# Kernel tuning notes

Hardware: AMD Instinct MI355X
Metric: run time of the kernel (lower is better)

The kernel has to match this reference:

```python
import jax, jax.numpy as jnp
import numpy as np

BN_EPS = 1e-5

def _bn(x, g, b):
    # BatchNorm1d, training-mode batch statistics
    mu = x.mean(axis=0)
    var = x.var(axis=0)
    return g * (x - mu) / jnp.sqrt(var + BN_EPS) + b

def setup_inputs() -> dict:
    key = jax.random.key(0)
    ks = jax.random.split(key, 10)
    B2, D_in, D1, DIMS, C = 16384, 1024, 512, 256, 40
    B = B2 // 2
    def w(k, shape, fan_in):
        return jax.random.normal(k, shape, jnp.float32) / np.float32(np.sqrt(fan_in))
    return {
        "lufeat": jax.random.normal(ks[0], (B2, D_in), jnp.float32),
        "llabel": jax.random.randint(ks[1], (B,), 0, C),
        "W1": w(ks[2], (D_in, D1), D_in), "b1": jnp.zeros(D1, jnp.float32),
        "W2": w(ks[3], (D1, DIMS), D1), "b2": jnp.zeros(DIMS, jnp.float32),
        "W3": w(ks[4], (DIMS + C, 256), DIMS + C), "b3": jnp.zeros(256, jnp.float32),
        "W4": w(ks[5], (256, 64), 256), "b4": jnp.zeros(64, jnp.float32),
        "W5": w(ks[6], (64, 1), 64), "b5": jnp.zeros(1, jnp.float32),
        "g1": jnp.ones(256, jnp.float32), "be1": jnp.zeros(256, jnp.float32),
        "g2": jnp.ones(64, jnp.float32), "be2": jnp.zeros(64, jnp.float32),
        "mbank0": jax.random.normal(ks[7], (C, DIMS), jnp.float32),
        "start0": jnp.zeros(C, jnp.float32),
    }

def reference(lufeat, llabel, W1, b1, W2, b2, W3, b3, W4, b4, W5, b5,
              g1, be1, g2, be2, mbank0, start0):
    B = lufeat.shape[0] // 2
    h = (lufeat @ W1 + b1) @ W2 + b2            # [2B, dims]
    h = h / jnp.linalg.norm(h, axis=1, keepdims=True)
    lfeat, ufeat = h[:B], h[B:]

    # Sequential per-sample memory-bank scatter/EMA update (detached feats)
    lf_sg = jax.lax.stop_gradient(lfeat)
    def step(carry, xs):
        start, mbank = carry
        lab, feat = xs
        row = jnp.where(start[lab] == 0, feat, 0.9 * mbank[lab] + 0.1 * feat)
        return (start.at[lab].set(1.0), mbank.at[lab].set(row)), None
    (_, mbank), _ = jax.lax.scan(step, (start0, mbank0), (llabel, lf_sg))
    mbank = jax.lax.stop_gradient(mbank)

    # cdist retrieval: [B, C] euclidean distances
    lm = jnp.linalg.norm(lfeat[:, None, :] - mbank[None, :, :], axis=-1)
    lscores = lm.min(axis=-1)
    um = jnp.linalg.norm(ufeat[:, None, :] - mbank[None, :, :], axis=-1)

    uf = jnp.concatenate([ufeat, um], axis=-1)   # [B, dims + C]
    u = jax.nn.relu(_bn(uf @ W3 + b3, g1, be1))
    u = jax.nn.relu(_bn(u @ W4 + b4, g2, be2))   # dropout = identity (eval)
    uscores = u @ W5 + b5                        # [B, 1]
    return lscores, uscores, mbank
```

## Files before the change

### kernel.cpp

```cpp
#include <hip/hip_runtime.h>
#include <hip/hip_bf16.h>
#include <stdint.h>

typedef __attribute__((ext_vector_type(4))) float f32x4;
typedef __attribute__((ext_vector_type(8))) short s16x8;
typedef __attribute__((ext_vector_type(4))) unsigned short u16x4;
typedef __attribute__((ext_vector_type(4))) int i32x4;

#define B2T 16384
#define BH 8192
#define DIN 1024
#define DD1 512
#define DIMS 256
#define NC 40
#define CAPS 2048

__device__ __forceinline__ unsigned short f2b(float f) {
  unsigned int u = __builtin_bit_cast(unsigned int, f);
  u += 0x7FFFu + ((u >> 16) & 1u);
  return (unsigned short)(u >> 16);
}

__device__ __forceinline__ float b2f(unsigned short u) {
  return __builtin_bit_cast(float, ((unsigned int)u) << 16);
}

__device__ __forceinline__ void gload16(const void* g, void* l) {
  __builtin_amdgcn_global_load_lds(
      (const __attribute__((address_space(1))) void*)g,
      (__attribute__((address_space(3))) void*)l, 16, 0, 0);
}

__global__ __launch_bounds__(256) void prep_all(const float* __restrict__ lufeat,
                                                unsigned short* __restrict__ lufeatH,
                                                const float* __restrict__ W1,
                                                const float* __restrict__ W2,
                                                const float* __restrict__ b1,
                                                const float* __restrict__ b2,
                                                const float* __restrict__ W3,
                                                const float* __restrict__ W4,
                                                unsigned short* __restrict__ WeffT,
                                                float* __restrict__ beff,
                                                unsigned short* __restrict__ W3T,
                                                unsigned short* __restrict__ W4T,
                                                float* __restrict__ statz) {
  __shared__ float W1s[32][36];
  __shared__ float W2sT[32][36];
  int b = blockIdx.x, t = threadIdx.x;
  if (b < 1024) {
#pragma unroll
    for (int i = 0; i < 8; ++i) {
      int idx = b * 16384 + i * 2048 + t * 8;
      f32x4 v0 = *(const f32x4*)(lufeat + idx);
      f32x4 v1 = *(const f32x4*)(lufeat + idx + 4);
      s16x8 p;
      p[0] = (short)f2b(v0[0]); p[1] = (short)f2b(v0[1]);
      p[2] = (short)f2b(v0[2]); p[3] = (short)f2b(v0[3]);
      p[4] = (short)f2b(v1[0]); p[5] = (short)f2b(v1[1]);
      p[6] = (short)f2b(v1[2]); p[7] = (short)f2b(v1[3]);
      *(s16x8*)(lufeatH + idx) = p;
    }
  } else if (b < 1280) {
    int bb = b - 1024;
    int k0 = (bb & 31) * 32, n0 = (bb >> 5) * 32;
    int nn = t & 31, kq = t >> 5;
    f32x4 acc = (f32x4){0.f, 0.f, 0.f, 0.f};
    for (int j0 = 0; j0 < DD1; j0 += 32) {
#pragma unroll
      for (int i = 0; i < 4; ++i) {
        int idx = t + 256 * i;
        int kk = idx >> 5, jj = idx & 31;
        W1s[kk][jj] = W1[(size_t)(k0 + kk) * DD1 + j0 + jj];
        W2sT[jj][kk] = W2[(size_t)(j0 + kk) * DIMS + n0 + jj];
      }
      __syncthreads();
#pragma unroll
      for (int jj4 = 0; jj4 < 8; ++jj4) {
        f32x4 w2 = *(const f32x4*)&W2sT[nn][jj4 * 4];
        f32x4 w1_0 = *(const f32x4*)&W1s[kq * 4 + 0][jj4 * 4];
        f32x4 w1_1 = *(const f32x4*)&W1s[kq * 4 + 1][jj4 * 4];
        f32x4 w1_2 = *(const f32x4*)&W1s[kq * 4 + 2][jj4 * 4];
        f32x4 w1_3 = *(const f32x4*)&W1s[kq * 4 + 3][jj4 * 4];
        acc[0] += w1_0[0] * w2[0] + w1_0[1] * w2[1] + w1_0[2] * w2[2] + w1_0[3] * w2[3];
        acc[1] += w1_1[0] * w2[0] + w1_1[1] * w2[1] + w1_1[2] * w2[2] + w1_1[3] * w2[3];
        acc[2] += w1_2[0] * w2[0] + w1_2[1] * w2[1] + w1_2[2] * w2[2] + w1_2[3] * w2[3];
        acc[3] += w1_3[0] * w2[0] + w1_3[1] * w2[1] + w1_3[2] * w2[2] + w1_3[3] * w2[3];
      }
      __syncthreads();
    }
    u16x4 pk = {f2b(acc[0]), f2b(acc[1]), f2b(acc[2]), f2b(acc[3])};
    *(u16x4*)(WeffT + (size_t)(n0 + nn) * DIN + k0 + kq * 4) = pk;
  } else if (b == 1280) {
    float a0 = 0.f, a1 = 0.f, a2 = 0.f, a3 = 0.f, a4 = 0.f, a5 = 0.f, a6 = 0.f, a7 = 0.f;
    for (int j = 0; j < DD1; j += 8) {
      a0 += b1[j + 0] * W2[(size_t)(j + 0) * DIMS + t];
      a1 += b1[j + 1] * W2[(size_t)(j + 1) * DIMS + t];
      a2 += b1[j + 2] * W2[(size_t)(j + 2) * DIMS + t];
      a3 += b1[j + 3] * W2[(size_t)(j + 3) * DIMS + t];
      a4 += b1[j + 4] * W2[(size_t)(j + 4) * DIMS + t];
      a5 += b1[j + 5] * W2[(size_t)(j + 5) * DIMS + t];
      a6 += b1[j + 6] * W2[(size_t)(j + 6) * DIMS + t];
      a7 += b1[j + 7] * W2[(size_t)(j + 7) * DIMS + t];
    }
    beff[t] = b2[t] + (((a0 + a1) + (a2 + a3)) + ((a4 + a5) + (a6 + a7)));
  } else if (b < 1601) {
    int idx = (b - 1281) * 256 + t;
    int n = idx / 320, k = idx - n * 320;
    float v = (k < 296) ? W3[(size_t)k * 256 + n] : 0.0f;
    W3T[(size_t)n * 320 + k] = f2b(v);
  } else if (b < 1665) {
    int idx = (b - 1601) * 256 + t;
    int n = idx >> 8, k = idx & 255;
    W4T[(size_t)n * 256 + k] = f2b(W4[(size_t)k * 64 + n]);
  } else {
    for (int i = t; i < 680; i += 256) statz[i] = 0.0f;
  }
}

__global__ __launch_bounds__(256) void gemm1_dma(
    const unsigned short* __restrict__ AH, const unsigned short* __restrict__ BT,
    const float* __restrict__ bias, float* __restrict__ C,
    unsigned short* __restrict__ uf) {
  __shared__ __align__(16) char A_s[2][4096];
  __shared__ __align__(16) char B_s[2][32768];
  __shared__ float rs[4][32];
  int t = threadIdx.x, m0 = blockIdx.x * 32;
  int w = t >> 6, lane = t & 63, q = lane >> 4, ln = lane & 15;
  f32x4 acc[2][4];
#pragma unroll
  for (int mi = 0; mi < 2; ++mi)
// ... 84 lines not shown
      int ribf = mi * 16 + q * 4 + r;
      float inv = rs[0][ribf];
      int grow = m0 + ribf;
#pragma unroll
      for (int ni = 0; ni < 4; ++ni) {
        int col = w * 64 + ni * 16 + ln;
        float nv = v[mi][ni][r] * inv;
        if (grow < BH)
          C[(size_t)grow * DIMS + col] = nv;
        else
          uf[(size_t)(grow - BH) * 320 + col] = f2b(nv);
      }
    }
}

template <int AMODE, int NB, int MI, int CW, int EPI, int K, int TPB>
__global__ __launch_bounds__(TPB) void gemm_core(
    const void* __restrict__ Aptr, int lda, const unsigned short* __restrict__ BT,
    const float* __restrict__ bias, float* __restrict__ C, int ldc,
    float* __restrict__ sums, float* __restrict__ ssqs,
    const float* __restrict__ bnsum, const float* __restrict__ bnssq,
    const float* __restrict__ bng, const float* __restrict__ bnbe,
    unsigned short* __restrict__ uf) {
  constexpr int NW = TPB / 64;
  constexpr int RG = NW / CW;
  constexpr int AR = RG * MI * 16;
  constexpr int ACH = AR * 8;
  constexpr int ABN = (ACH + TPB - 1) / TPB;
  constexpr int BBN = NB * 8 / TPB;
  constexpr int BBUF = NB * 128;
  constexpr int ALOADS = (AMODE == 1) ? ABN : 2 * ABN;
  constexpr bool UNIF = (ACH >= TPB);
  __shared__ __align__(16) short A_s[2][AR][72];
  __shared__ __align__(16) char B_s[2 * BBUF];
  __shared__ float rs[CW][AR];
  __shared__ float bsc_s[(AMODE == 2) ? 256 : 1];
  __shared__ float bsh_s[(AMODE == 2) ? 256 : 1];
  int t = threadIdx.x;
  int m0 = blockIdx.x * AR;
  int w = t >> 6, lane = t & 63, q = lane >> 4, ln = lane & 15;
  f32x4 acc[MI][4];
#pragma unroll
  for (int mi = 0; mi < MI; ++mi)
#pragma unroll
    for (int ni = 0; ni < 4; ++ni) acc[mi][ni] = (f32x4){0.f, 0.f, 0.f, 0.f};

  f32x4 pa0[ABN][2], pa1[ABN][2];
  s16x8 pab0[ABN], pab1[ABN];

  auto issue = [&](int kbase, f32x4 (&paX)[ABN][2], s16x8 (&pabX)[ABN]) {
    if (ACH >= TPB || t < ACH) {
#pragma unroll
      for (int i = 0; i < ABN; ++i) {
        int ch = t + TPB * i, row = ch >> 3, kp = (ch & 7) * 8;
        if constexpr (AMODE == 1) {
          const unsigned short* A = (const unsigned short*)Aptr;
          pabX[i] = *(const s16x8*)(A + (size_t)(m0 + row) * lda + kbase + kp);
        } else {
          const float* A = (const float*)Aptr;
          const f32x4* src = (const f32x4*)(A + (size_t)(m0 + row) * lda + kbase + kp);
          paX[i][0] = src[0];
          paX[i][1] = src[1];
        }
      }
    }
  };

  auto gloadB = [&](int kbase, int bufi) {
#pragma unroll
    for (int i = 0; i < BBN; ++i) {
      int ch = t + TPB * i;
      int n = ch >> 3, j = ch & 7;
      int ksw = (j ^ (n & 7)) * 8;
      gload16(BT + (size_t)n * K + kbase + ksw,
              B_s + bufi * BBUF + (w * 64 + TPB * i) * 16);
    }
  };

  auto stage = [&](int kk, int bufi, f32x4 (&paX)[ABN][2], s16x8 (&pabX)[ABN]) {
    if (ACH >= TPB || t < ACH) {
#pragma unroll
      for (int i = 0; i < ABN; ++i) {
        int ch = t + TPB * i, row = ch >> 3, kp = (ch & 7) * 8;
        if constexpr (AMODE == 1) {
          *(s16x8*)&A_s[bufi][row][kp] = pabX[i];
        } else {
          f32x4 v0 = paX[i][0], v1 = paX[i][1];
          if constexpr (AMODE == 2) {
            float vv[8] = {v0[0], v0[1], v0[2], v0[3], v1[0], v1[1], v1[2], v1[3]};
#pragma unroll
            for (int j = 0; j < 8; ++j) {
              int f = kk + kp + j;
              vv[j] = fmaxf(vv[j] * bsc_s[f] + bsh_s[f], 0.0f);
            }
            v0 = (f32x4){vv[0], vv[1], vv[2], vv[3]};
            v1 = (f32x4){vv[4], vv[5], vv[6], vv[7]};
          }
          s16x8 p;
          p[0] = (short)f2b(v0[0]); p[1] = (short)f2b(v0[1]);
          p[2] = (short)f2b(v0[2]); p[3] = (short)f2b(v0[3]);
          p[4] = (short)f2b(v1[0]); p[5] = (short)f2b(v1[1]);
          p[6] = (short)f2b(v1[2]); p[7] = (short)f2b(v1[3]);
          *(s16x8*)&A_s[bufi][row][kp] = p;
        }
      }
    }
  };

  auto compute = [&](int cur) {
#pragma unroll
    for (int k32 = 0; k32 < 64; k32 += 32) {
      s16x8 af[MI];
      int ab = (w / CW) * MI * 16;
#pragma unroll
      for (int mi = 0; mi < MI; ++mi)
        af[mi] = *(const s16x8*)&A_s[cur][ab + mi * 16 + ln][k32 + q * 8];
      int nb0 = (w % CW) * 64;
#pragma unroll
      for (int ni = 0; ni < 4; ++ni) {
        int brow = nb0 + ni * 16 + ln;
        int bb = (brow * 128 + (k32 + q * 8) * 2) ^ ((brow & 7) << 4);
        s16x8 bfr = *(const s16x8*)(B_s + cur * BBUF + bb);
#pragma unroll
        for (int mi = 0; mi < MI; ++mi)
          acc[mi][ni] = __builtin_amdgcn_mfma_f32_16x16x32_bf16(af[mi], bfr, acc[mi][ni], 0, 0, 0);
      }
    }
  };

  auto kbar = [&](bool keepA) {
    if constexpr (UNIF) {
      if (keepA)
        asm volatile("s_waitcnt vmcnt(%0) lgkmcnt(0)" ::"n"(ALOADS) : "memory");
      else
        asm volatile("s_waitcnt vmcnt(0) lgkmcnt(0)" ::: "memory");
      __builtin_amdgcn_s_barrier();
      __builtin_amdgcn_sched_barrier(0);
    } else {
      __syncthreads();
    }
  };

  if constexpr (AMODE == 2) {
    if (t < 256) {
      float mu = bnsum[t] * (1.0f / 8192.0f);
      float var = bnssq[t] * (1.0f / 8192.0f) - mu * mu;
      float sc = bng[t] * rsqrtf(var + 1e-5f);
      bsc_s[t] = sc;
      bsh_s[t] = bnbe[t] - mu * sc;
    }
    __syncthreads();
  }

  const int nst = K >> 6;
  issue(0, pa0, pab0);
  gloadB(0, 0);
  __builtin_amdgcn_sched_barrier(0);
  if (nst > 1) issue(64, pa1, pab1);
  stage(0, 0, pa0, pab0);
  kbar(nst > 1);

  for (int s = 0; s < nst; s += 2) {
    if (s + 1 < nst) gloadB((s + 1) << 6, 1);
    __builtin_amdgcn_sched_barrier(0);
    if (s + 2 < nst) issue((s + 2) << 6, pa0, pab0);
    compute(0);
    if (s + 1 < nst) stage((s + 1) << 6, 1, pa1, pab1);
    kbar(s + 2 < nst);
    if (s + 1 < nst) {
      if (s + 2 < nst) gloadB((s + 2) << 6, 0);
      __builtin_amdgcn_sched_barrier(0);
      if (s + 3 < nst) issue((s + 3) << 6, pa1, pab1);
      compute(1);
      if (s + 2 < nst) stage((s + 2) << 6, 0, pa0, pab0);
      kbar(s + 3 < nst);
    }
  }

  float v[MI][4][4];
#pragma unroll
  for (int mi = 0; mi < MI; ++mi)
#pragma unroll
    for (int ni = 0; ni < 4; ++ni) {
      float bv = bias[(w % CW) * 64 + ni * 16 + ln];
#pragma unroll
      for (int r = 0; r < 4; ++r) v[mi][ni][r] = acc[mi][ni][r] + bv;
    }

#pragma unroll
  for (int mi = 0; mi < MI; ++mi)
#pragma unroll
    for (int ni = 0; ni < 4; ++ni)
#pragma unroll
      for (int r = 0; r < 4; ++r) {
        int grow = m0 + (w / CW) * MI * 16 + mi * 16 + q * 4 + r;
        int col = (w % CW) * 64 + ni * 16 + ln;
        C[(size_t)grow * ldc + col] = v[mi][ni][r];
      }
  if constexpr (EPI == 2 || EPI == 3) {
#pragma unroll
    for (int ni = 0; ni < 4; ++ni) {
      float s = 0.f, s2 = 0.f;
#pragma unroll
      for (int mi = 0; mi < MI; ++mi)
#pragma unroll
        for (int r = 0; r < 4; ++r) {
          float x = v[mi][ni][r];
          s += x; s2 += x * x;
        }
      s += __shfl_xor(s, 16); s += __shfl_xor(s, 32);
      s2 += __shfl_xor(s2, 16); s2 += __shfl_xor(s2, 32);
      if (q == 0) {
        int col = (w % CW) * 64 + ni * 16 + ln;
        atomicAdd(&sums[col], s);
        atomicAdd(&ssqs[col], s2);
      }
    }
  }
}

__global__ __launch_bounds__(256) void bank_kernel(const int* __restrict__ llabel,
                                                   const float* __restrict__ Hn,
                                                   const float* __restrict__ mbank0,
                                                   const float* __restrict__ start0,
                                                   float* __restrict__ mbank_out,
                                                   float* __restrict__ msq) {
  __shared__ i32x4 lab4[BH / 4];
  __shared__ int idx_s[CAPS];
  __shared__ float redp[256];
  __shared__ int wcnt[4];
  int t = threadIdx.x, c = blockIdx.x >> 2, dq = blockIdx.x & 3;
  int w = t >> 6, lane = t & 63;
  const float l09 = -0.15200309344504997f;

  for (int i = t; i < BH / 4; i += 256) lab4[i] = ((const i32x4*)llabel)[i];
  __syncthreads();
  const int* lab_s = (const int*)lab4;

  int base0 = w * (BH / 4);
  int cnt = 0;
  for (int b = 0; b < BH / 4; b += 64)
    cnt += (int)__popcll(__ballot(lab_s[base0 + b + lane] == c));
  if (lane == 0) wcnt[w] = cnt;
  __syncthreads();
  int off = 0;
#pragma unroll
  for (int i = 0; i < 4; ++i)
    if (i < w) off += wcnt[i];
  int Ktot = wcnt[0] + wcnt[1] + wcnt[2] + wcnt[3];
  int running = off;
  for (int b = 0; b < BH / 4; b += 64) {
    bool hit = lab_s[base0 + b + lane] == c;
    unsigned long long mk = __ballot(hit);
    if (hit) {
      int pos = running + (int)__popcll(mk & ((1ull << lane) - 1ull));
      if (pos < CAPS) idx_s[pos] = base0 + b + lane;
    }
    running += (int)__popcll(mk);
  }
  __syncthreads();
  int K = Ktot < CAPS ? Ktot : CAPS;
  bool fresh = (start0[c] == 0.0f);
  int dcol = t & 63, rr = t >> 6;
  int d = dq * 64 + dcol;
  float p0 = 0.f, p1 = 0.f, p2 = 0.f, p3 = 0.f;
  if (K > 0) {
    float w0fold = fresh ? exp2f((float)K * l09) : 0.f;
    int m = rr;
    for (; m + 12 < K; m += 16) {
      float e = (float)(K - 1 - m);
      float wa = 0.1f * exp2f(e * l09) + (m == 0 ? w0fold : 0.f);
      p0 += wa * Hn[(size_t)idx_s[m] * DIMS + d];
      p1 += 0.1f * exp2f((e - 4.f) * l09) * Hn[(size_t)idx_s[m + 4] * DIMS + d];
      p2 += 0.1f * exp2f((e - 8.f) * l09) * Hn[(size_t)idx_s[m + 8] * DIMS + d];
      p3 += 0.1f * exp2f((e - 12.f) * l09) * Hn[(size_t)idx_s[m + 12] * DIMS + d];
    }
    for (; m < K; m += 4) {
      float wa = 0.1f * exp2f((float)(K - 1 - m) * l09) + (m == 0 ? w0fold : 0.f);
      p0 += wa * Hn[(size_t)idx_s[m] * DIMS + d];
    }
  }
  redp[rr * 64 + dcol] = (p0 + p1) + (p2 + p3);
  __syncthreads();
  if (t < 64) {
    int dd = dq * 64 + t;
    float out;
    if (K == 0) {
      out = mbank0[(size_t)c * DIMS + dd];
    } else {
      float base_v = fresh ? 0.f : exp2f((float)K * l09) * mbank0[(size_t)c * DIMS + dd];
      out = ((redp[t] + redp[64 + t]) + (redp[128 + t] + redp[192 + t])) + base_v;
    }
    mbank_out[(size_t)c * DIMS + dd] = out;
    float vv = out * out;
#pragma unroll
    for (int o = 32; o; o >>= 1) vv += __shfl_xor(vv, o);
    if (t == 0) atomicAdd(&msq[c], vv);
  }
}

__global__ __launch_bounds__(256) void dist_kernel(const float* __restrict__ Hn,
                                                   const float* __restrict__ mbank,
                                                   const float* __restrict__ msq,
                                                   float* __restrict__ lscores,
                                                   unsigned short* __restrict__ uf) {
  __shared__ float Ms[NC][260];
  __shared__ float Hs[32][260];
  __shared__ float msq_s[NC];
  int t = threadIdx.x;
  int r0 = blockIdx.x * 32;
  for (int e = t; e < NC * 64; e += 256) {
    int i = e >> 6, d0 = (e & 63) * 4;
    *(f32x4*)&Ms[i][d0] = *(const f32x4*)(mbank + (size_t)i * DIMS + d0);
  }
  if (r0 < BH) {
    for (int e = t; e < 32 * 64; e += 256) {
      int i = e >> 6, d0 = (e & 63) * 4;
      *(f32x4*)&Hs[i][d0] = *(const f32x4*)(Hn + (size_t)(r0 + i) * DIMS + d0);
    }
  } else {
    for (int e = t; e < 32 * 32; e += 256) {
      int i = e >> 5, d0 = (e & 31) * 8;
      s16x8 vb = *(const s16x8*)(uf + (size_t)(r0 - BH + i) * 320 + d0);
#pragma unroll
      for (int j = 0; j < 8; ++j) Hs[i][d0 + j] = b2f((unsigned short)vb[j]);
    }
  }
  if (t < NC) msq_s[t] = msq[t];
  __syncthreads();
  int r = t >> 3, c0 = (t & 7) * 5;
  float g0 = 0, g1 = 0, g2 = 0, g3 = 0, g4 = 0;
  for (int d = 0; d < DIMS; d += 4) {
    f32x4 f = *(const f32x4*)&Hs[r][d];
    f32x4 m0v = *(const f32x4*)&Ms[c0 + 0][d];
    f32x4 m1v = *(const f32x4*)&Ms[c0 + 1][d];
    f32x4 m2v = *(const f32x4*)&Ms[c0 + 2][d];
    f32x4 m3v = *(const f32x4*)&Ms[c0 + 3][d];
    f32x4 m4v = *(const f32x4*)&Ms[c0 + 4][d];
    g0 += f[0] * m0v[0] + f[1] * m0v[1] + f[2] * m0v[2] + f[3] * m0v[3];
    g1 += f[0] * m1v[0] + f[1] * m1v[1] + f[2] * m1v[2] + f[3] * m1v[3];
    g2 += f[0] * m2v[0] + f[1] * m2v[1] + f[2] * m2v[2] + f[3] * m2v[3];
    g3 += f[0] * m3v[0] + f[1] * m3v[1] + f[2] * m3v[2] + f[3] * m3v[3];
    g4 += f[0] * m4v[0] + f[1] * m4v[1] + f[2] * m4v[2] + f[3] * m4v[3];
  }
  int row = r0 + r;
  float d2[5];
  d2[0] = 1.0f + msq_s[c0 + 0] - 2.0f * g0;
  d2[1] = 1.0f + msq_s[c0 + 1] - 2.0f * g1;
  d2[2] = 1.0f + msq_s[c0 + 2] - 2.0f * g2;
  d2[3] = 1.0f + msq_s[c0 + 3] - 2.0f * g3;
  d2[4] = 1.0f + msq_s[c0 + 4] - 2.0f * g4;
  if (row < BH) {
    float mn = fminf(fminf(fminf(d2[0], d2[1]), fminf(d2[2], d2[3])), d2[4]);
    mn = fminf(mn, __shfl_xor(mn, 1, 8));
    mn = fminf(mn, __shfl_xor(mn, 2, 8));
    mn = fminf(mn, __shfl_xor(mn, 4, 8));
    if ((t & 7) == 0) lscores[row] = sqrtf(fmaxf(mn, 0.0f));
  } else {
    unsigned short* dst = uf + (size_t)(row - BH) * 320 + 256 + c0;
#pragma unroll
    for (int qq = 0; qq < 5; ++qq) dst[qq] = f2b(sqrtf(fmaxf(d2[qq], 0.0f)));
  }
}

__global__ __launch_bounds__(256) void uscore_bn(const float* __restrict__ y2,
                                                 const float* __restrict__ sums2,
                                                 const float* __restrict__ ssqs2,
                                                 const float* __restrict__ g2,
                                                 const float* __restrict__ be2,
                                                 const float* __restrict__ W5,
                                                 const float* __restrict__ b5,
                                                 float* __restrict__ out) {
  int t = threadIdx.x;
  int wv = t >> 6, lane = t & 63;
  int row = blockIdx.x * 4 + wv;
  float mu = sums2[lane] * (1.0f / 8192.0f);
  float var = ssqs2[lane] * (1.0f / 8192.0f) - mu * mu;
  float sc = g2[lane] * rsqrtf(var + 1e-5f);
  float sh = be2[lane] - mu * sc;
  float v = fmaxf(y2[(size_t)row * 64 + lane] * sc + sh, 0.0f) * W5[lane];
#pragma unroll
  for (int o = 32; o; o >>= 1) v += __shfl_xor(v, o);
  if (lane == 0) out[row] = v + b5[0];
}

extern "C" void kernel_launch(void* const* d_in, const int* in_sizes, int n_in,
                              void* d_out, int out_size, void* d_ws, size_t ws_size,
                              hipStream_t stream) {
  const float* lufeat = (const float*)d_in[0];
  const int* llabel = (const int*)d_in[1];
  const float* W1 = (const float*)d_in[2];
  const float* b1 = (const float*)d_in[3];
  const float* W2 = (const float*)d_in[4];
  const float* b2 = (const float*)d_in[5];
  const float* W3 = (const float*)d_in[6];
  const float* b3 = (const float*)d_in[7];
  const float* W4 = (const float*)d_in[8];
  const float* b4 = (const float*)d_in[9];
// ... 8 lines not shown

  char* ws = (char*)d_ws;
  unsigned short* WeffT = (unsigned short*)(ws + 0);
  float* Hraw = (float*)(ws + 524288);
  float* ybuf = (float*)(ws + 524288);
  float* y2 = (float*)(ws + 8912896);
  unsigned short* uf = (unsigned short*)(ws + 17301504);
  unsigned short* W3T = (unsigned short*)(ws + 22544384);
  unsigned short* W4T = (unsigned short*)(ws + 22708224);
  float* beff = (float*)(ws + 22740992);
  float* sums1 = (float*)(ws + 22742016);
  float* ssq1 = sums1 + 256;
  float* sums2 = ssq1 + 256;
  float* ssq2 = sums2 + 64;
  float* msq = (float*)(ws + 22744576);
  unsigned short* lufeatH = (unsigned short*)(ws + 25165824);

  float* lscores = (float*)d_out;
  float* uscores = lscores + 8192;
  float* mbank = uscores + 8192;

  prep_all<<<1666, 256, 0, stream>>>(lufeat, lufeatH, W1, W2, b1, b2, W3, W4,
                                     WeffT, beff, W3T, W4T, sums1);
  gemm1_dma<<<512, 256, 0, stream>>>(lufeatH, WeffT, beff, Hraw, uf);
  bank_kernel<<<160, 256, 0, stream>>>(llabel, Hraw, mbank0, start0, mbank, msq);
  dist_kernel<<<512, 256, 0, stream>>>(Hraw, mbank, msq, lscores, uf);
  gemm_core<1, 256, 1, 4, 2, 320, 512><<<256, 512, 0, stream>>>(
      uf, 320, W3T, b3, ybuf, 256,
      sums1, ssq1, nullptr, nullptr, nullptr, nullptr, nullptr);
  gemm_core<2, 64, 1, 1, 3, 256, 256><<<128, 256, 0, stream>>>(
      ybuf, 256, W4T, b4, y2, 64,
      sums2, ssq2, sums1, ssq1, g1, be1, nullptr);
  uscore_bn<<<2048, 256, 0, stream>>>(y2, sums2, ssq2, g2, be2, W5, b5, uscores);
}
```

Before: 238.2 us.

## Fuse post-GEMM stages into one persistent kernel with atomic flag barriers

Replaces the bank, distance, two GEMM and uscore launches with a single back_all kernel. Block ranges take on each stage and wait on global atomic counters that earlier-stage blocks increment after a release fence. The flags live in workspace and are zeroed by the enlarged statz clear in prep_all. This removes several launch gaps and tail effects, but it relies on earlier-stage blocks being scheduled before the waiting ones (deadlock risk), and the GEMM tiles are retuned with smaller M per block. The prep kernel is also reordered so the small weight-prep blocks are dispatched before the large bf16 conversion.

```diff
diff --git a/kernel.cpp b/kernel.cpp
--- a/kernel.cpp
+++ b/kernel.cpp
@@ -29,6 +29,21 @@
   __builtin_amdgcn_global_load_lds(
       (const __attribute__((address_space(1))) void*)g,
       (__attribute__((address_space(3))) void*)l, 16, 0, 0);
+}
+
+__device__ __forceinline__ void sig(unsigned* f) {
+  __builtin_amdgcn_fence(__ATOMIC_RELEASE, "agent");
+  __syncthreads();
+  if (threadIdx.x == 0)
+    __hip_atomic_fetch_add(f, 1u, __ATOMIC_RELAXED, __HIP_MEMORY_SCOPE_AGENT);
+}
+__device__ __forceinline__ void waitf(unsigned* f, unsigned n) {
+  if (threadIdx.x == 0) {
+    while (__hip_atomic_load(f, __ATOMIC_RELAXED, __HIP_MEMORY_SCOPE_AGENT) < n)
+      __builtin_amdgcn_s_sleep(32);
+  }
+  __syncthreads();
+  __builtin_amdgcn_fence(__ATOMIC_ACQUIRE, "agent");
 }
 
 __global__ __launch_bounds__(256) void prep_all(const float* __restrict__ lufeat,
@@ -47,22 +62,8 @@
   __shared__ float W1s[32][36];
   __shared__ float W2sT[32][36];
   int b = blockIdx.x, t = threadIdx.x;
-  if (b < 1024) {
-#pragma unroll
-    for (int i = 0; i < 8; ++i) {
-      int idx = b * 16384 + i * 2048 + t * 8;
-      f32x4 v0 = *(const f32x4*)(lufeat + idx);
-      f32x4 v1 = *(const f32x4*)(lufeat + idx + 4);
-      s16x8 p;
-      p[0] = (short)f2b(v0[0]); p[1] = (short)f2b(v0[1]);
-      p[2] = (short)f2b(v0[2]); p[3] = (short)f2b(v0[3]);
-      p[4] = (short)f2b(v1[0]); p[5] = (short)f2b(v1[1]);
-      p[6] = (short)f2b(v1[2]); p[7] = (short)f2b(v1[3]);
-      *(s16x8*)(lufeatH + idx) = p;
-    }
-  } else if (b < 1280) {
-    int bb = b - 1024;
-    int k0 = (bb & 31) * 32, n0 = (bb >> 5) * 32;
+  if (b < 256) {
+    int k0 = (b & 31) * 32, n0 = (b >> 5) * 32;
     int nn = t & 31, kq = t >> 5;
     f32x4 acc = (f32x4){0.f, 0.f, 0.f, 0.f};
     for (int j0 = 0; j0 < DD1; j0 += 32) {
@@ -90,7 +91,7 @@
     }
     u16x4 pk = {f2b(acc[0]), f2b(acc[1]), f2b(acc[2]), f2b(acc[3])};
     *(u16x4*)(WeffT + (size_t)(n0 + nn) * DIN + k0 + kq * 4) = pk;
-  } else if (b == 1280) {
+  } else if (b == 256) {
     float a0 = 0.f, a1 = 0.f, a2 = 0.f, a3 = 0.f, a4 = 0.f, a5 = 0.f, a6 = 0.f, a7 = 0.f;
     for (int j = 0; j < DD1; j += 8) {
       a0 += b1[j + 0] * W2[(size_t)(j + 0) * DIMS + t];
@@ -103,17 +104,31 @@
       a7 += b1[j + 7] * W2[(size_t)(j + 7) * DIMS + t];
     }
     beff[t] = b2[t] + (((a0 + a1) + (a2 + a3)) + ((a4 + a5) + (a6 + a7)));
-  } else if (b < 1601) {
-    int idx = (b - 1281) * 256 + t;
+  } else if (b < 577) {
+    int idx = (b - 257) * 256 + t;
     int n = idx / 320, k = idx - n * 320;
     float v = (k < 296) ? W3[(size_t)k * 256 + n] : 0.0f;
     W3T[(size_t)n * 320 + k] = f2b(v);
-  } else if (b < 1665) {
-    int idx = (b - 1601) * 256 + t;
+  } else if (b < 641) {
+    int idx = (b - 577) * 256 + t;
     int n = idx >> 8, k = idx & 255;
     W4T[(size_t)n * 256 + k] = f2b(W4[(size_t)k * 64 + n]);
+  } else if (b == 641) {
+    for (int i = t; i < 684; i += 256) statz[i] = 0.0f;
   } else {
-    for (int i = t; i < 680; i += 256) statz[i] = 0.0f;
+    size_t base = (size_t)(b - 642) * 16384 + (size_t)t * 8;
+#pragma unroll
+    for (int i = 0; i < 8; ++i) {
+      size_t idx = base + (size_t)i * 2048;
+      f32x4 v0 = *(const f32x4*)(lufeat + idx);
+      f32x4 v1 = *(const f32x4*)(lufeat + idx + 4);
+      s16x8 p;
+      p[0] = (short)f2b(v0[0]); p[1] = (short)f2b(v0[1]);
+      p[2] = (short)f2b(v0[2]); p[3] = (short)f2b(v0[3]);
+      p[4] = (short)f2b(v1[0]); p[5] = (short)f2b(v1[1]);
+      p[6] = (short)f2b(v1[2]); p[7] = (short)f2b(v1[3]);
+      *(s16x8*)(lufeatH + idx) = p;
+    }
   }
 }
 
@@ -228,374 +243,332 @@
     }
 }
 
-template <int AMODE, int NB, int MI, int CW, int EPI, int K, int TPB>
-__global__ __launch_bounds__(TPB) void gemm_core(
-    const void* __restrict__ Aptr, int lda, const unsigned short* __restrict__ BT,
-    const float* __restrict__ bias, float* __restrict__ C, int ldc,
-    float* __restrict__ sums, float* __restrict__ ssqs,
-    const float* __restrict__ bnsum, const float* __restrict__ bnssq,
-    const float* __restrict__ bng, const float* __restrict__ bnbe,
-    unsigned short* __restrict__ uf) {
-  constexpr int NW = TPB / 64;
-  constexpr int RG = NW / CW;
-  constexpr int AR = RG * MI * 16;
-  constexpr int ACH = AR * 8;
-  constexpr int ABN = (ACH + TPB - 1) / TPB;
-  constexpr int BBN = NB * 8 / TPB;
-  constexpr int BBUF = NB * 128;
-  constexpr int ALOADS = (AMODE == 1) ? ABN : 2 * ABN;
-  constexpr bool UNIF = (ACH >= TPB);
-  __shared__ __align__(16) short A_s[2][AR][72];
-  __shared__ __align__(16) char B_s[2 * BBUF];
-  __shared__ float rs[CW][AR];
-  __shared__ float bsc_s[(AMODE == 2) ? 256 : 1];
-  __shared__ float bsh_s[(AMODE == 2) ? 256 : 1];
-  int t = threadIdx.x;
-  int m0 = blockIdx.x * AR;
-  int w = t >> 6, lane = t & 63, q = lane >> 4, ln = lane & 15;
-  f32x4 acc[MI][4];
-#pragma unroll
-  for (int mi = 0; mi < MI; ++mi)
-#pragma unroll
-    for (int ni = 0; ni < 4; ++ni) acc[mi][ni] = (f32x4){0.f, 0.f, 0.f, 0.f};
-
-  f32x4 pa0[ABN][2], pa1[ABN][2];
-  s16x8 pab0[ABN], pab1[ABN];
-
-  auto issue = [&](int kbase, f32x4 (&paX)[ABN][2], s16x8 (&pabX)[ABN]) {
-    if (ACH >= TPB || t < ACH) {
-#pragma unroll
-      for (int i = 0; i < ABN; ++i) {
-        int ch = t + TPB * i, row = ch >> 3, kp = (ch & 7) * 8;
-        if constexpr (AMODE == 1) {
-          const unsigned short* A = (const unsigned short*)Aptr;
-          pabX[i] = *(const s16x8*)(A + (size_t)(m0 + row) * lda + kbase + kp);
-        } else {
-          const float* A = (const float*)Aptr;
-          const f32x4* src = (const f32x4*)(A + (size_t)(m0 + row) * lda + kbase + kp);
-          paX[i][0] = src[0];
-          paX[i][1] = src[1];
+__global__ __launch_bounds__(256) void back_all(
+    const int* llabel, const float* Hn, const float* mbank0, const float* start0,
+    float* mbank, float* msq, float* lscores, unsigned short* uf,
+    const unsigned short* W3T, const float* b3, float* ybuf,
+    float* sums1, float* ssq1, const float* g1, const float* be1,
+    const unsigned short* W4T, const float* b4, float* y2,
+    float* sums2, float* ssq2, const float* g2, const float* be2,
+    const float* W5, const float* b5, float* uscores, unsigned* flags) {
+  __shared__ __align__(16) char smem[75264];
+  const int bx = blockIdx.x, t = threadIdx.x;
+  const int w = t >> 6, lane = t & 63, q = lane >> 4, ln = lane & 15;
+  const float l09 = -0.15200309344504997f;
+
+  if (bx < 160) {
+    int c = bx >> 2, dq = bx & 3;
+    int* lab_s = (int*)smem;
+    int* idx_s = (int*)(smem + 32768);
+    float* redp = (float*)(smem + 40960);
+    int* wcnt = (int*)(smem + 41984);
+    for (int i = t; i < BH / 4; i += 256) ((i32x4*)lab_s)[i] = ((const i32x4*)llabel)[i];
+    __syncthreads();
+    int base0 = w * (BH / 4);
+    int cnt = 0;
+    for (int b = 0; b < BH / 4; b += 64)
+      cnt += (int)__popcll(__ballot(lab_s[base0 + b + lane] == c));
+    if (lane == 0) wcnt[w] = cnt;
+    __syncthreads();
+    int off = 0;
+#pragma unroll
+    for (int i = 0; i < 4; ++i)
+      if (i < w) off += wcnt[i];
+    int Ktot = wcnt[0] + wcnt[1] + wcnt[2] + wcnt[3];
+    int running = off;
+    for (int b = 0; b < BH / 4; b += 64) {
+      bool hit = lab_s[base0 + b + lane] == c;
+      unsigned long long mk = __ballot(hit);
+      if (hit) {
+        int pos = running + (int)__popcll(mk & ((1ull << lane) - 1ull));
+        if (pos < CAPS) idx_s[pos] = base0 + b + lane;
+      }
+      running += (int)__popcll(mk);
+    }
+    __syncthreads();
+    int K = Ktot < CAPS ? Ktot : CAPS;
+    bool fresh = (start0[c] == 0.0f);
+    int dcol = t & 63, rr = t >> 6;
+    int d = dq * 64 + dcol;
+    float p0 = 0.f, p1 = 0.f, p2 = 0.f, p3 = 0.f;
+    if (K > 0) {
+      float w0fold = fresh ? exp2f((float)K * l09) : 0.f;
+      int m = rr;
+      for (; m + 12 < K; m += 16) {
+        float e = (float)(K - 1 - m);
+        float wa = 0.1f * exp2f(e * l09) + (m == 0 ? w0fold : 0.f);
+        p0 += wa * Hn[(size_t)idx_s[m] * DIMS + d];
+        p1 += 0.1f * exp2f((e - 4.f) * l09) * Hn[(size_t)idx_s[m + 4] * DIMS + d];
+        p2 += 0.1f * exp2f((e - 8.f) * l09) * Hn[(size_t)idx_s[m + 8] * DIMS + d];
+        p3 += 0.1f * exp2f((e - 12.f) * l09) * Hn[(size_t)idx_s[m + 12] * DIMS + d];
+      }
+      for (; m < K; m += 4) {
+        float wa = 0.1f * exp2f((float)(K - 1 - m) * l09) + (m == 0 ? w0fold : 0.f);
+        p0 += wa * Hn[(size_t)idx_s[m] * DIMS + d];
+      }
+    }
+    redp[rr * 64 + dcol] = (p0 + p1) + (p2 + p3);
+    __syncthreads();
+    if (t < 64) {
+      int dd = dq * 64 + t;
+      float out;
+      if (K == 0) {
+        out = mbank0[(size_t)c * DIMS + dd];
+      } else {
+        float base_v = fresh ? 0.f : exp2f((float)K * l09) * mbank0[(size_t)c * DIMS + dd];
+        out = ((redp[t] + redp[64 + t]) + (redp[128 + t] + redp[192 + t])) + base_v;
+      }
+      mbank[(size_t)c * DIMS + dd] = out;
+      float vv = out * out;
+#pragma unroll
+      for (int o = 32; o; o >>= 1) vv += __shfl_xor(vv, o);
+      if (t == 0) atomicAdd(&msq[c], vv);
+    }
+    sig(flags + 0);
+  } else if (bx < 672) {
+    waitf(flags + 0, 160u);
+    int db = bx - 160;
+    float* Ms = (float*)smem;
+    float* Hs = (float*)(smem + 41600);
+    float* msq_s = (float*)(smem + 74880);
+    int r0 = db * 32;
+    for (int e = t; e < NC * 64; e += 256) {
+      int i = e >> 6, d0 = (e & 63) * 4;
+      *(f32x4*)&Ms[i * 260 + d0] = *(const f32x4*)(mbank + (size_t)i * DIMS + d0);
+    }
+    if (r0 < BH) {
+      for (int e = t; e < 32 * 64; e += 256) {
+        int i = e >> 6, d0 = (e & 63) * 4;
+        *(f32x4*)&Hs[i * 260 + d0] = *(const f32x4*)(Hn + (size_t)(r0 + i) * DIMS + d0);
+      }
+    } else {
+      for (int e = t; e < 32 * 32; e += 256) {
+        int i = e >> 5, d0 = (e & 31) * 8;
+        s16x8 vb = *(const s16x8*)(uf + (size_t)(r0 - BH + i) * 320 + d0);
+#pragma unroll
+        for (int j = 0; j < 8; ++j) Hs[i * 260 + d0 + j] = b2f((unsigned short)vb[j]);
+      }
+    }
+    if (t < NC) msq_s[t] = msq[t];
+    __syncthreads();
+    int r = t >> 3, c0 = (t & 7) * 5;
+    float g0 = 0, g1v = 0, g2v = 0, g3 = 0, g4 = 0;
+    for (int d = 0; d < DIMS; d += 4) {
+      f32x4 f = *(const f32x4*)&Hs[r * 260 + d];
+      f32x4 m0v = *(const f32x4*)&Ms[(c0 + 0) * 260 + d];
+      f32x4 m1v = *(const f32x4*)&Ms[(c0 + 1) * 260 + d];
+      f32x4 m2v = *(const f32x4*)&Ms[(c0 + 2) * 260 + d];
+      f32x4 m3v = *(const f32x4*)&Ms[(c0 + 3) * 260 + d];
+      f32x4 m4v = *(const f32x4*)&Ms[(c0 + 4) * 260 + d];
+      g0 += f[0] * m0v[0] + f[1] * m0v[1] + f[2] * m0v[2] + f[3] * m0v[3];
+      g1v += f[0] * m1v[0] + f[1] * m1v[1] + f[2] * m1v[2] + f[3] * m1v[3];
+      g2v += f[0] * m2v[0] + f[1] * m2v[1] + f[2] * m2v[2] + f[3] * m2v[3];
+      g3 += f[0] * m3v[0] + f[1] * m3v[1] + f[2] * m3v[2] + f[3] * m3v[3];
+      g4 += f[0] * m4v[0] + f[1] * m4v[1] + f[2] * m4v[2] + f[3] * m4v[3];
+    }
+    int row = r0 + r;
+    float d2[5];
+    d2[0] = 1.0f + msq_s[c0 + 0] - 2.0f * g0;
+    d2[1] = 1.0f + msq_s[c0 + 1] - 2.0f * g1v;
+    d2[2] = 1.0f + msq_s[c0 + 2] - 2.0f * g2v;
+    d2[3] = 1.0f + msq_s[c0 + 3] - 2.0f * g3;
+    d2[4] = 1.0f + msq_s[c0 + 4] - 2.0f * g4;
+    if (row < BH) {
+      float mn = fminf(fminf(fminf(d2[0], d2[1]), fminf(d2[2], d2[3])), d2[4]);
+      mn = fminf(mn, __shfl_xor(mn, 1, 8));
+      mn = fminf(mn, __shfl_xor(mn, 2, 8));
+      mn = fminf(mn, __shfl_xor(mn, 4, 8));
+      if ((t & 7) == 0) lscores[row] = sqrtf(fmaxf(mn, 0.0f));
+    } else {
+      unsigned short* dst = uf + (size_t)(row - BH) * 320 + 256 + c0;
+#pragma unroll
+      for (int qq = 0; qq < 5; ++qq) dst[qq] = f2b(sqrtf(fmaxf(d2[qq], 0.0f)));
+    }
+    sig(flags + 1);
+  } else if (bx < 1184) {
+    waitf(flags + 1, 512u);
+    int gb = bx - 672;
+    char* A_s = smem;
+    char* B_s = smem + 4096;
+    int m0 = gb * 16;
+    f32x4 acc[4];
+#pragma unroll
+    for (int ni = 0; ni < 4; ++ni) acc[ni] = (f32x4){0.f, 0.f, 0.f, 0.f};
+
+    auto dma = [&](int s, int bufi) {
+      int kb = s * 64;
+      if (t < 128) {
+        int row = t >> 3, j = t & 7;
+        gload16(uf + (size_t)(m0 + row) * 320 + kb + ((j ^ (row & 7)) * 8),
+                A_s + bufi * 2048 + t * 16);
+      }
+#pragma unroll
+      for (int i = 0; i < 8; ++i) {
+        int ch = t + 256 * i, n = ch >> 3, j = ch & 7;
+        gload16(W3T + (size_t)n * 320 + kb + ((j ^ (n & 7)) * 8),
+                B_s + bufi * 32768 + (w * 64 + 256 * i) * 16);
+      }
+    };
+    auto compute = [&](int bufi) {
+#pragma unroll
+      for (int k32 = 0; k32 < 64; k32 += 32) {
+        int koff = (k32 + q * 8) * 2;
+        int arow = ln;
+        s16x8 af = *(const s16x8*)(A_s + bufi * 2048 + ((arow * 128 + koff) ^ ((arow & 7) << 4)));
+        int nb0 = w * 64;
+#pragma unroll
+        for (int ni = 0; ni < 4; ++ni) {
+          int brow = nb0 + ni * 16 + ln;
+          s16x8 bfr = *(const s16x8*)(B_s + bufi * 32768 + ((brow * 128 + koff) ^ ((brow & 7) << 4)));
+          acc[ni] = __builtin_amdgcn_mfma_f32_16x16x32_bf16(af, bfr, acc[ni], 0, 0, 0);
         }
       }
-    }
-  };
-
-  auto gloadB = [&](int kbase, int bufi) {
-#pragma unroll
-    for (int i = 0; i < BBN; ++i) {
-      int ch = t + TPB * i;
-      int n = ch >> 3, j = ch & 7;
-      int ksw = (j ^ (n & 7)) * 8;
-      gload16(BT + (size_t)n * K + kbase + ksw,
-              B_s + bufi * BBUF + (w * 64 + TPB * i) * 16);
-    }
-  };
-
-  auto stage = [&](int kk, int bufi, f32x4 (&paX)[ABN][2], s16x8 (&pabX)[ABN]) {
-    if (ACH >= TPB || t < ACH) {
-#pragma unroll
-      for (int i = 0; i < ABN; ++i) {
-        int ch = t + TPB * i, row = ch >> 3, kp = (ch & 7) * 8;
-        if constexpr (AMODE == 1) {
-          *(s16x8*)&A_s[bufi][row][kp] = pabX[i];
-        } else {
-          f32x4 v0 = paX[i][0], v1 = paX[i][1];
-          if constexpr (AMODE == 2) {
-            float vv[8] = {v0[0], v0[1], v0[2], v0[3], v1[0], v1[1], v1[2], v1[3]};
-#pragma unroll
-            for (int j = 0; j < 8; ++j) {
-              int f = kk + kp + j;
-              vv[j] = fmaxf(vv[j] * bsc_s[f] + bsh_s[f], 0.0f);
-            }
-            v0 = (f32x4){vv[0], vv[1], vv[2], vv[3]};
-            v1 = (f32x4){vv[4], vv[5], vv[6], vv[7]};
-          }
-          s16x8 p;
-          p[0] = (short)f2b(v0[0]); p[1] = (short)f2b(v0[1]);
-          p[2] = (short)f2b(v0[2]); p[3] = (short)f2b(v0[3]);
-          p[4] = (short)f2b(v1[0]); p[5] = (short)f2b(v1[1]);
-          p[6] = (short)f2b(v1[2]); p[7] = (short)f2b(v1[3]);
-          *(s16x8*)&A_s[bufi][row][kp] = p;
-        }
-      }
-    }
-  };
-
-  auto compute = [&](int cur) {
-#pragma unroll
-    for (int k32 = 0; k32 < 64; k32 += 32) {
-      s16x8 af[MI];
-      int ab = (w / CW) * MI * 16;
-#pragma unroll
-      for (int mi = 0; mi < MI; ++mi)
-        af[mi] = *(const s16x8*)&A_s[cur][ab + mi * 16 + ln][k32 + q * 8];
-      int nb0 = (w % CW) * 64;
-#pragma unroll
-      for (int ni = 0; ni < 4; ++ni) {
-        int brow = nb0 + ni * 16 + ln;
-        int bb = (brow * 128 + (k32 + q * 8) * 2) ^ ((brow & 7) << 4);
-        s16x8 bfr = *(const s16x8*)(B_s + cur * BBUF + bb);
-#pragma unroll
-        for (int mi = 0; mi < MI; ++mi)
-          acc[mi][ni] = __builtin_amdgcn_mfma_f32_16x16x32_bf16(af[mi], bfr, acc[mi][ni], 0, 0, 0);
-      }
-    }
-  };
-
-  auto kbar = [&](bool keepA) {
-    if constexpr (UNIF) {
-      if (keepA)
-        asm volatile("s_waitcnt vmcnt(%0) lgkmcnt(0)" ::"n"(ALOADS) : "memory");
-      else
-        asm volatile("s_waitcnt vmcnt(0) lgkmcnt(0)" ::: "memory");
-      __builtin_amdgcn_s_barrier();
-      __builtin_amdgcn_sched_barrier(0);
-    } else {
+    };
+    dma(0, 0);
+    __syncthreads();
+    for (int s = 0; s < 5; ++s) {
+      if (s + 1 < 5) dma(s + 1, (s + 1) & 1);
+      compute(s & 1);
       __syncthreads();
     }
-  };
-
-  if constexpr (AMODE == 2) {
-    if (t < 256) {
-      float mu = bnsum[t] * (1.0f / 8192.0f);
-      float var = bnssq[t] * (1.0f / 8192.0f) - mu * mu;
-      float sc = bng[t] * rsqrtf(var + 1e-5f);
-      bsc_s[t] = sc;
-      bsh_s[t] = bnbe[t] - mu * sc;
-    }
-    __syncthreads();
-  }
-
-  const int nst = K >> 6;
-  issue(0, pa0, pab0);
-  gloadB(0, 0);
-  __builtin_amdgcn_sched_barrier(0);
-  if (nst > 1) issue(64, pa1, pab1);
-  stage(0, 0, pa0, pab0);
-  kbar(nst > 1);
-
-  for (int s = 0; s < nst; s += 2) {
-    if (s + 1 < nst) gloadB((s + 1) << 6, 1);
-    __builtin_amdgcn_sched_barrier(0);
-    if (s + 2 < nst) issue((s + 2) << 6, pa0, pab0);
-    compute(0);
-    if (s + 1 < nst) stage((s + 1) << 6, 1, pa1, pab1);
-    kbar(s + 2 < nst);
-    if (s + 1 < nst) {
-      if (s + 2 < nst) gloadB((s + 2) << 6, 0);
-      __builtin_amdgcn_sched_barrier(0);
-      if (s + 3 < nst) issue((s + 3) << 6, pa1, pab1);
-      compute(1);
-      if (s + 2 < nst) stage((s + 2) << 6, 0, pa0, pab0);
-      kbar(s + 3 < nst);
-    }
-  }
-
-  float v[MI][4][4];
-#pragma unroll
-  for (int mi = 0; mi < MI; ++mi)
 #pragma unroll
     for (int ni = 0; ni < 4; ++ni) {
-      float bv = bias[(w % CW) * 64 + ni * 16 + ln];
-#pragma unroll
-      for (int r = 0; r < 4; ++r) v[mi][ni][r] = acc[mi][ni][r] + bv;
-    }
-
-#pragma unroll
-  for (int mi = 0; mi < MI; ++mi)
-#pragma unroll
-    for (int ni = 0; ni < 4; ++ni)
+      int col = w * 64 + ni * 16 + ln;
+      float bv = b3[col];
+      float s = 0.f, s2 = 0.f;
 #pragma unroll
       for (int r = 0; r < 4; ++r) {
-        int grow = m0 + (w / CW) * MI * 16 + mi * 16 + q * 4 + r;
-        int col = (w % CW) * 64 + ni * 16 + ln;
-        C[(size_t)grow * ldc + col] = v[mi][ni][r];
-      }
-  if constexpr (EPI == 2 || EPI == 3) {
-#pragma unroll
-    for (int ni = 0; ni < 4; ++ni) {
-      float s = 0.f, s2 = 0.f;
-#pragma unroll
-      for (int mi = 0; mi < MI; ++mi)
-#pragma unroll
-        for (int r = 0; r < 4; ++r) {
-          float x = v[mi][ni][r];
-          s += x; s2 += x * x;
-        }
+        float x = acc[ni][r] + bv;
+        ybuf[(size_t)(m0 + q * 4 + r) * 256 + col] = x;
+        s += x; s2 += x * x;
+      }
       s += __shfl_xor(s, 16); s += __shfl_xor(s, 32);
       s2 += __shfl_xor(s2, 16); s2 += __shfl_xor(s2, 32);
       if (q == 0) {
-        int col = (w % CW) * 64 + ni * 16 + ln;
-        atomicAdd(&sums[col], s);
-        atomicAdd(&ssqs[col], s2);
-      }
+        atomicAdd(&sums1[col], s);
+        atomicAdd(&ssq1[col], s2);
+      }
+    }
+    sig(flags + 2);
+  } else if (bx < 1312) {
+    waitf(flags + 2, 512u);
+    int hb = bx - 1184;
+    short* A3 = (short*)smem;
+    char* B3 = smem + 18432;
+    float* bsc = (float*)(smem + 34816);
+    float* bsh = (float*)(smem + 35840);
+    {
+      float mu = sums1[t] * (1.0f / 8192.0f);
+      float var = ssq1[t] * (1.0f / 8192.0f) - mu * mu;
+      float sc = g1[t] * rsqrtf(var + 1e-5f);
+      bsc[t] = sc;
+      bsh[t] = be1[t] - mu * sc;
+    }
+    __syncthreads();
+    int m0 = hb * 64;
+    f32x4 acc[4];
+#pragma unroll
+    for (int ni = 0; ni < 4; ++ni) acc[ni] = (f32x4){0.f, 0.f, 0.f, 0.f};
+    f32x4 pa0[2][2], pa1[2][2];
+    auto issueA3 = [&](int kbase, f32x4 (&pa)[2][2]) {
+#pragma unroll
+      for (int i = 0; i < 2; ++i) {
+        int ch = t + 256 * i, row = ch >> 3, kp = (ch & 7) * 8;
+        const f32x4* src = (const f32x4*)(ybuf + (size_t)(m0 + row) * 256 + kbase + kp);
+        pa[i][0] = src[0];
+        pa[i][1] = src[1];
+      }
+    };
+    auto stageA3 = [&](int kbase, int bufi, f32x4 (&pa)[2][2]) {
+#pragma unroll
+      for (int i = 0; i < 2; ++i) {
+        int ch = t + 256 * i, row = ch >> 3, kp = (ch & 7) * 8;
+        float vv[8] = {pa[i][0][0], pa[i][0][1], pa[i][0][2], pa[i][0][3],
+                       pa[i][1][0], pa[i][1][1], pa[i][1][2], pa[i][1][3]};
+#pragma unroll
+        for (int j = 0; j < 8; ++j) {
+          int f = kbase + kp + j;
+          vv[j] = fmaxf(vv[j] * bsc[f] + bsh[f], 0.0f);
+        }
+        s16x8 p;
+        p[0] = (short)f2b(vv[0]); p[1] = (short)f2b(vv[1]);
+        p[2] = (short)f2b(vv[2]); p[3] = (short)f2b(vv[3]);
+        p[4] = (short)f2b(vv[4]); p[5] = (short)f2b(vv[5]);
+        p[6] = (short)f2b(vv[6]); p[7] = (short)f2b(vv[7]);
+        *(s16x8*)&A3[(bufi * 64 + row) * 72 + kp] = p;
+      }
+    };
+    auto gloadB3 = [&](int kbase, int bufi) {
+#pragma unroll
+      for (int i = 0; i < 2; ++i) {
+        int ch = t + 256 * i, n = ch >> 3, j = ch & 7;
+        gload16(W4T + (size_t)n * 256 + kbase + ((j ^ (n & 7)) * 8),
+                B3 + bufi * 8192 + ch * 16);
+      }
+    };
+    auto compute3 = [&](int cur) {
+#pragma unroll
+      for (int k32 = 0; k32 < 64; k32 += 32) {
+        s16x8 af = *(const s16x8*)&A3[(cur * 64 + w * 16 + ln) * 72 + k32 + q * 8];
+#pragma unroll
+        for (int ni = 0; ni < 4; ++ni) {
+          int brow = ni * 16 + ln;
+          int bb = (brow * 128 + (k32 + q * 8) * 2) ^ ((brow & 7) << 4);
+          s16x8 bfr = *(const s16x8*)(B3 + cur * 8192 + bb);
+          acc[ni] = __builtin_amdgcn_mfma_f32_16x16x32_bf16(af, bfr, acc[ni], 0, 0, 0);
+        }
+      }
+    };
+    issueA3(0, pa0);
+    gloadB3(0, 0);
+    stageA3(0, 0, pa0);
+    issueA3(64, pa1);
+    __syncthreads();
+    for (int s = 0; s < 4; ++s) {
+      int cur = s & 1;
+      if (s + 1 < 4) gloadB3((s + 1) << 6, cur ^ 1);
+      if (s + 2 < 4) issueA3((s + 2) << 6, (s & 1) ? pa1 : pa0);
+      compute3(cur);
+      if (s + 1 < 4) stageA3((s + 1) << 6, cur ^ 1, (s & 1) ? pa0 : pa1);
+      __syncthreads();
+    }
+#pragma unroll
+    for (int ni = 0; ni < 4; ++ni) {
+      int col = ni * 16 + ln;
+      float bv = b4[col];
+      float s = 0.f, s2 = 0.f;
+#pragma unroll
+      for (int r = 0; r < 4; ++r) {
+        float x = acc[ni][r] + bv;
+        y2[(size_t)(m0 + w * 16 + q * 4 + r) * 64 + col] = x;
+        s += x; s2 += x * x;
+      }
+      s += __shfl_xor(s, 16); s += __shfl_xor(s, 32);
+      s2 += __shfl_xor(s2, 16); s2 += __shfl_xor(s2, 32);
+      if (q == 0) {
+        atomicAdd(&sums2[col], s);
+        atomicAdd(&ssq2[col], s2);
+      }
+    }
+    sig(flags + 3);
+  } else {
+    waitf(flags + 3, 128u);
+    int ub = bx - 1312;
+    float mu = sums2[lane] * (1.0f / 8192.0f);
+    float var = ssq2[lane] * (1.0f / 8192.0f) - mu * mu;
+    float sc = g2[lane] * rsqrtf(var + 1e-5f);
+    float sh = be2[lane] - mu * sc;
+    float w5 = W5[lane];
+    float bb5 = b5[0];
+#pragma unroll
+    for (int i = 0; i < 4; ++i) {
+      int row = ub * 16 + i * 4 + w;
+      float v = fmaxf(y2[(size_t)row * 64 + lane] * sc + sh, 0.0f) * w5;
+#pragma unroll
+      for (int o = 32; o; o >>= 1) v += __shfl_xor(v, o);
+      if (lane == 0) uscores[row] = v + bb5;
     }
   }
-}
-
-__global__ __launch_bounds__(256) void bank_kernel(const int* __restrict__ llabel,
-                                                   const float* __restrict__ Hn,
-                                                   const float* __restrict__ mbank0,
-                                                   const float* __restrict__ start0,
-                                                   float* __restrict__ mbank_out,
-                                                   float* __restrict__ msq) {
-  __shared__ i32x4 lab4[BH / 4];
-  __shared__ int idx_s[CAPS];
-  __shared__ float redp[256];
-  __shared__ int wcnt[4];
-  int t = threadIdx.x, c = blockIdx.x >> 2, dq = blockIdx.x & 3;
-  int w = t >> 6, lane = t & 63;
-  const float l09 = -0.15200309344504997f;
-
-  for (int i = t; i < BH / 4; i += 256) lab4[i] = ((const i32x4*)llabel)[i];
-  __syncthreads();
-  const int* lab_s = (const int*)lab4;
-
-  int base0 = w * (BH / 4);
-  int cnt = 0;
-  for (int b = 0; b < BH / 4; b += 64)
-    cnt += (int)__popcll(__ballot(lab_s[base0 + b + lane] == c));
-  if (lane == 0) wcnt[w] = cnt;
-  __syncthreads();
-  int off = 0;
-#pragma unroll
-  for (int i = 0; i < 4; ++i)
-    if (i < w) off += wcnt[i];
-  int Ktot = wcnt[0] + wcnt[1] + wcnt[2] + wcnt[3];
-  int running = off;
-  for (int b = 0; b < BH / 4; b += 64) {
-    bool hit = lab_s[base0 + b + lane] == c;
-    unsigned long long mk = __ballot(hit);
-    if (hit) {
-      int pos = running + (int)__popcll(mk & ((1ull << lane) - 1ull));
-      if (pos < CAPS) idx_s[pos] = base0 + b + lane;
-    }
-    running += (int)__popcll(mk);
-  }
-  __syncthreads();
-  int K = Ktot < CAPS ? Ktot : CAPS;
-  bool fresh = (start0[c] == 0.0f);
-  int dcol = t & 63, rr = t >> 6;
-  int d = dq * 64 + dcol;
-  float p0 = 0.f, p1 = 0.f, p2 = 0.f, p3 = 0.f;
-  if (K > 0) {
-    float w0fold = fresh ? exp2f((float)K * l09) : 0.f;
-    int m = rr;
-    for (; m + 12 < K; m += 16) {
-      float e = (float)(K - 1 - m);
-      float wa = 0.1f * exp2f(e * l09) + (m == 0 ? w0fold : 0.f);
-      p0 += wa * Hn[(size_t)idx_s[m] * DIMS + d];
-      p1 += 0.1f * exp2f((e - 4.f) * l09) * Hn[(size_t)idx_s[m + 4] * DIMS + d];
-      p2 += 0.1f * exp2f((e - 8.f) * l09) * Hn[(size_t)idx_s[m + 8] * DIMS + d];
-      p3 += 0.1f * exp2f((e - 12.f) * l09) * Hn[(size_t)idx_s[m + 12] * DIMS + d];
-    }
-    for (; m < K; m += 4) {
-      float wa = 0.1f * exp2f((float)(K - 1 - m) * l09) + (m == 0 ? w0fold : 0.f);
-      p0 += wa * Hn[(size_t)idx_s[m] * DIMS + d];
-    }
-  }
-  redp[rr * 64 + dcol] = (p0 + p1) + (p2 + p3);
-  __syncthreads();
-  if (t < 64) {
-    int dd = dq * 64 + t;
-    float out;
-    if (K == 0) {
-      out = mbank0[(size_t)c * DIMS + dd];
-    } else {
-      float base_v = fresh ? 0.f : exp2f((float)K * l09) * mbank0[(size_t)c * DIMS + dd];
-      out = ((redp[t] + redp[64 + t]) + (redp[128 + t] + redp[192 + t])) + base_v;
-    }
-    mbank_out[(size_t)c * DIMS + dd] = out;
-    float vv = out * out;
-#pragma unroll
-    for (int o = 32; o; o >>= 1) vv += __shfl_xor(vv, o);
-    if (t == 0) atomicAdd(&msq[c], vv);
-  }
-}
-
-__global__ __launch_bounds__(256) void dist_kernel(const float* __restrict__ Hn,
-                                                   const float* __restrict__ mbank,
-                                                   const float* __restrict__ msq,
-                                                   float* __restrict__ lscores,
-                                                   unsigned short* __restrict__ uf) {
-  __shared__ float Ms[NC][260];
-  __shared__ float Hs[32][260];
-  __shared__ float msq_s[NC];
-  int t = threadIdx.x;
-  int r0 = blockIdx.x * 32;
-  for (int e = t; e < NC * 64; e += 256) {
-    int i = e >> 6, d0 = (e & 63) * 4;
-    *(f32x4*)&Ms[i][d0] = *(const f32x4*)(mbank + (size_t)i * DIMS + d0);
-  }
-  if (r0 < BH) {
-    for (int e = t; e < 32 * 64; e += 256) {
-      int i = e >> 6, d0 = (e & 63) * 4;
-      *(f32x4*)&Hs[i][d0] = *(const f32x4*)(Hn + (size_t)(r0 + i) * DIMS + d0);
-    }
-  } else {
-    for (int e = t; e < 32 * 32; e += 256) {
-      int i = e >> 5, d0 = (e & 31) * 8;
-      s16x8 vb = *(const s16x8*)(uf + (size_t)(r0 - BH + i) * 320 + d0);
-#pragma unroll
-      for (int j = 0; j < 8; ++j) Hs[i][d0 + j] = b2f((unsigned short)vb[j]);
-    }
-  }
-  if (t < NC) msq_s[t] = msq[t];
-  __syncthreads();
-  int r = t >> 3, c0 = (t & 7) * 5;
-  float g0 = 0, g1 = 0, g2 = 0, g3 = 0, g4 = 0;
-  for (int d = 0; d < DIMS; d += 4) {
-    f32x4 f = *(const f32x4*)&Hs[r][d];
-    f32x4 m0v = *(const f32x4*)&Ms[c0 + 0][d];
-    f32x4 m1v = *(const f32x4*)&Ms[c0 + 1][d];
-    f32x4 m2v = *(const f32x4*)&Ms[c0 + 2][d];
-    f32x4 m3v = *(const f32x4*)&Ms[c0 + 3][d];
-    f32x4 m4v = *(const f32x4*)&Ms[c0 + 4][d];
-    g0 += f[0] * m0v[0] + f[1] * m0v[1] + f[2] * m0v[2] + f[3] * m0v[3];
-    g1 += f[0] * m1v[0] + f[1] * m1v[1] + f[2] * m1v[2] + f[3] * m1v[3];
-    g2 += f[0] * m2v[0] + f[1] * m2v[1] + f[2] * m2v[2] + f[3] * m2v[3];
-    g3 += f[0] * m3v[0] + f[1] * m3v[1] + f[2] * m3v[2] + f[3] * m3v[3];
-    g4 += f[0] * m4v[0] + f[1] * m4v[1] + f[2] * m4v[2] + f[3] * m4v[3];
-  }
-  int row = r0 + r;
-  float d2[5];
-  d2[0] = 1.0f + msq_s[c0 + 0] - 2.0f * g0;
-  d2[1] = 1.0f + msq_s[c0 + 1] - 2.0f * g1;
-  d2[2] = 1.0f + msq_s[c0 + 2] - 2.0f * g2;
-  d2[3] = 1.0f + msq_s[c0 + 3] - 2.0f * g3;
-  d2[4] = 1.0f + msq_s[c0 + 4] - 2.0f * g4;
-  if (row < BH) {
-    float mn = fminf(fminf(fminf(d2[0], d2[1]), fminf(d2[2], d2[3])), d2[4]);
-    mn = fminf(mn, __shfl_xor(mn, 1, 8));
-    mn = fminf(mn, __shfl_xor(mn, 2, 8));
-    mn = fminf(mn, __shfl_xor(mn, 4, 8));
-    if ((t & 7) == 0) lscores[row] = sqrtf(fmaxf(mn, 0.0f));
-  } else {
-    unsigned short* dst = uf + (size_t)(row - BH) * 320 + 256 + c0;
-#pragma unroll
-    for (int qq = 0; qq < 5; ++qq) dst[qq] = f2b(sqrtf(fmaxf(d2[qq], 0.0f)));
-  }
-}
-
-__global__ __launch_bounds__(256) void uscore_bn(const float* __restrict__ y2,
-                                                 const float* __restrict__ sums2,
-                                                 const float* __restrict__ ssqs2,
-                                                 const float* __restrict__ g2,
-                                                 const float* __restrict__ be2,
-                                                 const float* __restrict__ W5,
-                                                 const float* __restrict__ b5,
-                                                 float* __restrict__ out) {
-  int t = threadIdx.x;
-  int wv = t >> 6, lane = t & 63;
-  int row = blockIdx.x * 4 + wv;
-  float mu = sums2[lane] * (1.0f / 8192.0f);
-  float var = ssqs2[lane] * (1.0f / 8192.0f) - mu * mu;
-  float sc = g2[lane] * rsqrtf(var + 1e-5f);
-  float sh = be2[lane] - mu * sc;
-  float v = fmaxf(y2[(size_t)row * 64 + lane] * sc + sh, 0.0f) * W5[lane];
-#pragma unroll
-  for (int o = 32; o; o >>= 1) v += __shfl_xor(v, o);
-  if (lane == 0) out[row] = v + b5[0];
 }
 
 extern "C" void kernel_launch(void* const* d_in, const int* in_sizes, int n_in,
@@ -634,6 +607,7 @@
   float* sums2 = ssq1 + 256;
   float* ssq2 = sums2 + 64;
   float* msq = (float*)(ws + 22744576);
+  unsigned* flags = (unsigned*)(ws + 22744736);
   unsigned short* lufeatH = (unsigned short*)(ws + 25165824);
 
   float* lscores = (float*)d_out;
@@ -643,13 +617,9 @@
   prep_all<<<1666, 256, 0, stream>>>(lufeat, lufeatH, W1, W2, b1, b2, W3, W4,
                                      WeffT, beff, W3T, W4T, sums1);
   gemm1_dma<<<512, 256, 0, stream>>>(lufeatH, WeffT, beff, Hraw, uf);
-  bank_kernel<<<160, 256, 0, stream>>>(llabel, Hraw, mbank0, start0, mbank, msq);
-  dist_kernel<<<512, 256, 0, stream>>>(Hraw, mbank, msq, lscores, uf);
-  gemm_core<1, 256, 1, 4, 2, 320, 512><<<256, 512, 0, stream>>>(
-      uf, 320, W3T, b3, ybuf, 256,
-      sums1, ssq1, nullptr, nullptr, nullptr, nullptr, nullptr);
-  gemm_core<2, 64, 1, 1, 3, 256, 256><<<128, 256, 0, stream>>>(
-      ybuf, 256, W4T, b4, y2, 64,
-      sums2, ssq2, sums1, ssq1, g1, be1, nullptr);
-  uscore_bn<<<2048, 256, 0, stream>>>(y2, sums2, ssq2, g2, be2, W5, b5, uscores);
-}
+  back_all<<<1824, 256, 0, stream>>>(
+      llabel, Hraw, mbank0, start0, mbank, msq, lscores, uf,
+      W3T, b3, ybuf, sums1, ssq1, g1, be1,
+      W4T, b4, y2, sums2, ssq2, g2, be2,
+      W5, b5, uscores, flags);
+}
```

After: 412.5 us. 1.73x slower.
